# Performance work log

Hardware: AMD Instinct MI355X
Metric: run time of the kernel (lower is better)

The kernel has to match this reference:

```python
import jax, jax.numpy as jnp
import numpy as np

B, S, D, H, G = 2, 4096, 768, 12, 64
HD = D // H
W = 256              # one-sided window (attention_window=512); also the chunk size
NC = S // W
NEG = -1e9
SCALE = 1.0 / np.sqrt(HD)


def setup_inputs() -> dict:
    key = jax.random.key(0)
    ks = jax.random.split(key, 9)
    lin = lambda k: 0.02 * jax.random.normal(k, (D, D), dtype=jnp.float32)
    zb = lambda: jnp.zeros((D,), jnp.float32)
    return {
        "query": jax.random.normal(ks[0], (S, B, D), dtype=jnp.float32),
        # 0 = local token, -1 = global token (wrapper multiplies by -1 -> +1 = global in HF convention)
        "key_padding_mask": jnp.zeros((B, S), jnp.int32).at[:, :G].set(-1),
        "Wq": lin(ks[1]), "bq": zb(),
        "Wk": lin(ks[2]), "bk": zb(),
        "Wv": lin(ks[3]), "bv": zb(),
        "Wqg": lin(ks[4]), "bqg": zb(),
        "Wkg": lin(ks[5]), "bkg": zb(),
        "Wvg": lin(ks[6]), "bvg": zb(),
        "Wo": lin(ks[7]), "bo": zb(),
    }


def _heads(x):  # [B,S,D] -> [B,H,S,HD]
    return x.reshape(B, S, H, HD).transpose(0, 2, 1, 3)


def reference(query, key_padding_mask, Wq, bq, Wk, bk, Wv, bv,
              Wqg, bqg, Wkg, bkg, Wvg, bvg, Wo, bo):
    x = query.transpose(1, 0, 2)                      # [B,S,D]
    attn_mask = -key_padding_mask                     # wrapper: key_padding_mask * -1
    is_pad = attn_mask < 0                            # [B,S]
    is_glb = attn_mask > 0

    q = _heads(x @ Wq + bq) * SCALE                   # [B,H,S,HD]
    k = _heads(x @ Wk + bk)
    v = _heads(x @ Wv + bv)

    # ---- sliding-window scores via overlapping 3-chunk key blocks ----
    qc = q.reshape(B, H, NC, W, HD)
    blk_idx = jnp.arange(NC)[:, None] * W + jnp.arange(3 * W)[None, :]   # [NC,3W] into padded seq
    kpad = jnp.pad(k, ((0, 0), (0, 0), (W, W), (0, 0)))
    vpad = jnp.pad(v, ((0, 0), (0, 0), (W, W), (0, 0)))
    kblk = kpad[:, :, blk_idx]                        # [B,H,NC,3W,HD]
    vblk = vpad[:, :, blk_idx]
    local = jnp.einsum('bhcqd,bhckd->bhcqk', qc, kblk)  # [B,H,NC,W,3W]

    rel = jnp.arange(3 * W)[None, :] - jnp.arange(W)[:, None] - W        # key pos - query pos
    jpos = (jnp.arange(NC)[:, None, None] - 1) * W + jnp.arange(3 * W)[None, None, :]
    band_ok = (jnp.abs(rel)[None] <= W) & (jpos >= 0) & (jpos < S)       # [NC,W,3W]

    key_bad = is_pad | is_glb                         # pad keys masked; global keys handled separately
    kb_blk = jnp.pad(key_bad, ((0, 0), (W, W)), constant_values=True)[:, blk_idx]  # [B,NC,3W]
    ok = band_ok[None, None] & ~kb_blk[:, None, :, None, :]
    local = jnp.where(ok, local, NEG)

    # ---- all queries -> global keys (first G tokens), regular K/V ----
    gsc = jnp.einsum('bhqd,bhgd->bhqg', q, k[:, :, :G])                  # [B,H,S,G]

    scores = jnp.concatenate([gsc, local.reshape(B, H, S, 3 * W)], axis=-1)
    probs = jax.nn.softmax(scores, axis=-1)
    pg = probs[..., :G]
    pl = probs[..., G:].reshape(B, H, NC, W, 3 * W)

    out = jnp.einsum('bhcqk,bhckd->bhcqd', pl, vblk).reshape(B, H, S, HD)
    out = out + jnp.einsum('bhqg,bhgd->bhqd', pg, v[:, :, :G])

    # ---- global query rows: full attention with the dedicated global projections ----
    qg = (_heads(x @ Wqg + bqg) * SCALE)[:, :, :G]    # [B,H,G,HD]
    kg = _heads(x @ Wkg + bkg)
    vg = _heads(x @ Wvg + bvg)
    gq = jnp.einsum('bhgd,bhkd->bhgk', qg, kg)        # [B,H,G,S]
    gq = jnp.where(is_pad[:, None, None, :], NEG, gq)
    gp = jax.nn.softmax(gq, axis=-1)
    out = out.at[:, :, :G].set(jnp.einsum('bhgk,bhkd->bhgd', gp, vg))

    attn_out = out.transpose(0, 2, 1, 3).reshape(B, S, D)   # merge heads -> [B,S,D]
    attn_out = attn_out.transpose(1, 0, 2)                  # back to [S,B,D]
    return attn_out @ Wo + bo                               # wrapper's output Linear
```

## Files before the change

kernel.cpp:

```cpp
#include <hip/hip_runtime.h>
#include <hip/hip_bf16.h>
#include <cstdint>

#define BB 2
#define SS 4096
#define DD 768
#define HH 12
#define GG 64
#define WW 256

typedef __hip_bfloat16 bf16;
typedef unsigned short u16;
typedef __attribute__((ext_vector_type(8))) short short8v;
typedef __attribute__((ext_vector_type(4))) float floatx4;
typedef __attribute__((ext_vector_type(16))) float floatx16;

#define QSCALE 0.18033688011112042f

__device__ __forceinline__ float b2f(u16 u) {
  return __uint_as_float(((unsigned int)u) << 16);
}
__device__ __forceinline__ u16 f2bu(float f) {
  bf16 h = __float2bfloat16(f);
  return *reinterpret_cast<u16*>(&h);
}
__device__ __forceinline__ void async_copy16(const u16* g, u16* l) {
  __builtin_amdgcn_global_load_lds(
      (const __attribute__((address_space(1))) void*)g,
      (__attribute__((address_space(3))) void*)l, 16, 0, 0);
}

struct P7 { const void* p[7]; };

__global__ __launch_bounds__(256) void detect_dtype(const u16* __restrict__ q,
                                                    int* __restrict__ flag) {
  __shared__ int cnt;
  int tid = threadIdx.x;
  if (tid == 0) cnt = 0;
  __syncthreads();
  int bad = 0;
#pragma unroll
  for (int i = 0; i < 16; ++i) {
    float f = b2f(q[tid * 16 + i]);
    if (!isfinite(f) || fabsf(f) > 100.f) bad++;
  }
  atomicAdd(&cnt, bad);
  __syncthreads();
  if (tid == 0) *flag = (cnt > 256) ? 1 : 0;
}

__global__ __launch_bounds__(256) void prep(P7 wsrc, P7 bsrc,
                                            const void* __restrict__ qsrc,
                                            bf16* __restrict__ cWt,
                                            bf16* __restrict__ cB,
                                            bf16* __restrict__ cQ,
                                            const int* __restrict__ flag) {
  bool f32 = (*flag != 0);
  int z = blockIdx.z;
  if (z < 7) {
    __shared__ float tile[32][33];
    const void* src = wsrc.p[z];
    bf16* d = cWt + (size_t)z * DD * DD;
    int tx = threadIdx.x & 31, ty = threadIdx.x >> 5;
    int k0 = blockIdx.x * 32, n0 = blockIdx.y * 32;
#pragma unroll
    for (int i = 0; i < 32; i += 8) {
      int k = k0 + ty + i, n = n0 + tx;
      float v = f32 ? ((const float*)src)[(size_t)k * DD + n]
                    : b2f(((const u16*)src)[(size_t)k * DD + n]);
      tile[ty + i][tx] = v;
    }
    __syncthreads();
#pragma unroll
    for (int i = 0; i < 32; i += 8) {
      int n = n0 + ty + i, k = k0 + tx;
      d[(size_t)n * DD + k] = __float2bfloat16(tile[tx][ty + i]);
    }
  } else if (z == 7) {
    int bidx = blockIdx.x + 24 * blockIdx.y;
    const int nch = (BB * HH * SS * 64) / 8;
    u16* cQp = (u16*)cQ;
    for (int c = bidx * 256 + threadIdx.x; c < nch; c += 576 * 256) {
      int i = c * 8;
      if (f32) {
        const float* qs = (const float*)qsrc;
        float4 a = *(const float4*)(qs + i);
        float4 b = *(const float4*)(qs + i + 4);
        ushort4 o1 = make_ushort4(f2bu(a.x), f2bu(a.y), f2bu(a.z), f2bu(a.w));
        ushort4 o2 = make_ushort4(f2bu(b.x), f2bu(b.y), f2bu(b.z), f2bu(b.w));
        *(ushort4*)(cQp + i) = o1;
        *(ushort4*)(cQp + i + 4) = o2;
      } else {
        const u16* qs = (const u16*)qsrc;
        *(ushort4*)(cQp + i) = *(const ushort4*)(qs + i);
        *(ushort4*)(cQp + i + 4) = *(const ushort4*)(qs + i + 4);
      }
    }
  } else {
    int which = blockIdx.x;
    if (which >= 7 || blockIdx.y != 0) return;
    const void* s = bsrc.p[which];
    for (int j = threadIdx.x; j < DD; j += 256)
      cB[which * DD + j] =
          __float2bfloat16(f32 ? ((const float*)s)[j] : b2f(((const u16*)s)[j]));
  }
}

__device__ __forceinline__ short8v lda(u16 (*Ls)[64], int base, int lane, int kk) {
  int row = base + (lane & 31);
  int c = (kk >> 3) + (lane >> 5);
  return *(const short8v*)&Ls[row][((c ^ (row & 7)) << 3)];
}

__device__ __forceinline__ void gemm_core2(const u16* __restrict__ Xp,
                                           const u16* __restrict__ Wp, int bm,
                                           int bn, int tid, u16 (*As)[64],
                                           u16 (*Bs)[64], floatx16 (&acc)[2][2]) {
  int lane = tid & 63, w = tid >> 6;
  int wm = (w >> 1) * 64, wn = (w & 1) * 64;
  int r8 = lane >> 3;
  int sw = (((lane & 7) ^ (r8 & 7)) << 3);
  for (int k0 = 0; k0 < DD; k0 += 64) {
    __syncthreads();
#pragma unroll
    for (int j = 0; j < 4; ++j) {
      async_copy16(Wp + (size_t)(bn + w * 32 + j * 8 + r8) * DD + k0 + sw,
                   &As[w * 32 + j * 8][0]);
      async_copy16(Xp + (size_t)(bm + w * 32 + j * 8 + r8) * DD + k0 + sw,
                   &Bs[w * 32 + j * 8][0]);
    }
    __syncthreads();
#pragma unroll
    for (int kk = 0; kk < 64; kk += 16) {
      short8v a0 = lda(As, wn, lane, kk);
      short8v a1 = lda(As, wn + 32, lane, kk);
      short8v b0 = lda(Bs, wm, lane, kk);
      short8v b1 = lda(Bs, wm + 32, lane, kk);
      acc[0][0] = __builtin_amdgcn_mfma_f32_32x32x16_bf16(a0, b0, acc[0][0], 0, 0, 0);
      acc[0][1] = __builtin_amdgcn_mfma_f32_32x32x16_bf16(a0, b1, acc[0][1], 0, 0, 0);
      acc[1][0] = __builtin_amdgcn_mfma_f32_32x32x16_bf16(a1, b0, acc[1][0], 0, 0, 0);
      acc[1][1] = __builtin_amdgcn_mfma_f32_32x32x16_bf16(a1, b1, acc[1][1], 0, 0, 0);
    }
  }
}

__global__ __launch_bounds__(256, 4) void gemm5c(const bf16* __restrict__ Xb,
                                                 const bf16* __restrict__ Wt0,
                                                 const bf16* __restrict__ bset,
                                                 bf16* __restrict__ out0,
                                                 bf16* __restrict__ qgp) {
  __shared__ __align__(16) u16 SH[16384];
  u16 (*As)[64] = (u16(*)[64])SH;
  u16 (*Bs)[64] = (u16(*)[64])(SH + 8192);
  int tid = threadIdx.x, lane = tid & 63, w = tid >> 6;
  int orig = blockIdx.x;
  const int NWG = 5 * 384 + 6, qq = NWG >> 3, rr = NWG & 7;
  int xcd = orig & 7, idx = orig >> 3;
  int wg = (xcd < rr ? xcd * (qq + 1) : rr * (qq + 1) + (xcd - rr) * qq) + idx;
  int which, bm, bn;
  if (wg >= 1920) {
    which = 5; bm = 0; bn = (wg - 1920) * 128;
  } else {
    which = wg / 384;
    int rem = wg % 384;
    bm = (rem / 6) * 128;
    bn = (rem % 6) * 128;
  }
  const u16* Wp = (const u16*)Wt0 + (size_t)which * DD * DD;
  const u16* bias = (const u16*)bset + which * DD;
  int Sdim = (which == 5) ? GG : SS;
  u16* outp = (which == 5) ? (u16*)qgp
                           : (u16*)out0 + (size_t)which * BB * HH * SS * 64;
  float scale = (which == 0 || which == 5) ? QSCALE : 1.f;

  floatx16 acc[2][2];
#pragma unroll
  for (int i = 0; i < 2; ++i)
#pragma unroll
    for (int j = 0; j < 2; ++j) acc[i][j] = (floatx16)(0.f);
  gemm_core2((const u16*)Xb, Wp, bm, bn, tid, As, Bs, acc);

  if (which == 2 || which == 4) {
    const int TST = 132;
    u16* Ct = SH;
    int h0 = bn >> 6;
    int wm = (w >> 1) * 64;
    int wnl = w & 1;
    int s0 = bm >> 1;
#pragma unroll
    for (int p = 0; p < 2; ++p) {
      __syncthreads();
      if (wnl == p) {
#pragma unroll
        for (int nt = 0; nt < 2; ++nt)
#pragma unroll
          for (int mt = 0; mt < 2; ++mt)
#pragma unroll
            for (int g = 0; g < 4; ++g) {
              int ncl = nt * 32 + g * 8 + ((lane >> 5) << 2);
              ushort4 bi = *(const ushort4*)&bias[bn + p * 64 + ncl];
              int mrow = wm + mt * 32 + (lane & 31);
              Ct[(ncl + 0) * TST + mrow] = f2bu(acc[nt][mt][4 * g + 0] + b2f(bi.x));
              Ct[(ncl + 1) * TST + mrow] = f2bu(acc[nt][mt][4 * g + 1] + b2f(bi.y));
              Ct[(ncl + 2) * TST + mrow] = f2bu(acc[nt][mt][4 * g + 2] + b2f(bi.z));
              Ct[(ncl + 3) * TST + mrow] = f2bu(acc[nt][mt][4 * g + 3] + b2f(bi.w));
            }
      }
      __syncthreads();
#pragma unroll
      for (int j = 0; j < 4; ++j) {
        int c = j * 256 + tid;
        int ch = c & 7, rrow = c >> 3;
        int d = rrow >> 1, b = rrow & 1;
        const u16* row = &Ct[d * TST + b];
        ushort4 o1, o2;
        o1.x = row[(ch * 8 + 0) << 1];
        o1.y = row[(ch * 8 + 1) << 1];
        o1.z = row[(ch * 8 + 2) << 1];
        o1.w = row[(ch * 8 + 3) << 1];
        o2.x = row[(ch * 8 + 4) << 1];
        o2.y = row[(ch * 8 + 5) << 1];
        o2.z = row[(ch * 8 + 6) << 1];
        o2.w = row[(ch * 8 + 7) << 1];
        u16* dst = outp + ((size_t)(b * HH + h0 + p)) * (SS * 64) +
                   (size_t)d * SS + s0 + ch * 8;
        *(ushort4*)dst = o1;
        *(ushort4*)(dst + 4) = o2;
      }
    }
    return;
  }

  const int CST = 132;
  u16* Cs = SH;
  int wn = (w & 1) << 6, wmh = (w >> 1) << 5;
#pragma unroll
  for (int mt = 0; mt < 2; ++mt) {
    __syncthreads();
#pragma unroll
    for (int nt = 0; nt < 2; ++nt)
#pragma unroll
      for (int g = 0; g < 4; ++g) {
        int ncol = wn + nt * 32 + g * 8 + ((lane >> 5) << 2);
        ushort4 bi = *(const ushort4*)&bias[bn + ncol];
        int crow = wmh + (lane & 31);
        ushort4 o;
        o.x = f2bu((acc[nt][mt][4 * g + 0] + b2f(bi.x)) * scale);
        o.y = f2bu((acc[nt][mt][4 * g + 1] + b2f(bi.y)) * scale);
        o.z = f2bu((acc[nt][mt][4 * g + 2] + b2f(bi.z)) * scale);
        o.w = f2bu((acc[nt][mt][4 * g + 3] + b2f(bi.w)) * scale);
        *(ushort4*)&Cs[crow * CST + ncol] = o;
      }
    __syncthreads();
#pragma unroll
    for (int j = 0; j < 8; ++j) {
      int c = j * 256 + tid;
      int ch = c & 15, mh = c >> 4;
      int mloc = mh >> 1, hloc = mh & 1;
      int m = bm + ((mloc >> 5) << 6) + mt * 32 + (mloc & 31);
      int s = m >> 1, b = m & 1;
      int h = (bn >> 6) + hloc;
      ushort4 vv = *(const ushort4*)&Cs[mloc * CST + hloc * 64 + ch * 4];
      *(ushort4*)(outp + ((size_t)(b * HH + h) * Sdim + s) * 64 + ch * 4) = vv;
    }
  }
}

__global__ __launch_bounds__(256, 4) void gemm_out(const bf16* __restrict__ Xb,
                                                   const bf16* __restrict__ Wtb,
                                                   const bf16* __restrict__ biasb,
                                                   float* __restrict__ outv) {
  __shared__ __align__(16) u16 SH[16384];
  u16 (*As)[64] = (u16(*)[64])SH;
  u16 (*Bs)[64] = (u16(*)[64])(SH + 8192);
  float* Cf = (float*)SH;
  int tid = threadIdx.x, lane = tid & 63, w = tid >> 6;
  int wn = (w & 1) * 64;
  int orig = blockIdx.x;
  int wg = (orig & 7) * 48 + (orig >> 3);
  int bm = (wg / 6) * 128, bn = (wg % 6) * 128;
  floatx16 acc[2][2];
#pragma unroll
  for (int i = 0; i < 2; ++i)
#pragma unroll
    for (int j = 0; j < 2; ++j) acc[i][j] = (floatx16)(0.f);
  gemm_core2((const u16*)Xb, (const u16*)Wtb, bm, bn, tid, As, Bs, acc);
  const u16* bias = (const u16*)biasb;
#pragma unroll
  for (int p = 0; p < 2; ++p) {
    __syncthreads();
    if ((w >> 1) == p) {
#pragma unroll
      for (int mt = 0; mt < 2; ++mt) {
        int mloc = mt * 32 + (lane & 31);
#pragma unroll
        for (int nt = 0; nt < 2; ++nt)
#pragma unroll
          for (int g = 0; g < 4; ++g) {
            int nl = wn + nt * 32 + g * 8 + ((lane >> 5) << 2);
            ushort4 bi = *(const ushort4*)&bias[bn + nl];
            float4 o;
            o.x = acc[nt][mt][4 * g + 0] + b2f(bi.x);
            o.y = acc[nt][mt][4 * g + 1] + b2f(bi.y);
            o.z = acc[nt][mt][4 * g + 2] + b2f(bi.z);
            o.w = acc[nt][mt][4 * g + 3] + b2f(bi.w);
            int n4 = nl >> 2;
            *(float4*)&Cf[mloc * 128 + ((n4 ^ (mloc & 31)) << 2)] = o;
          }
      }
    }
    __syncthreads();
#pragma unroll
    for (int j = 0; j < 8; ++j) {
      int c = j * 256 + tid;
      int mloc = c >> 5, nch = c & 31;
      float4 v = *(const float4*)&Cf[mloc * 128 + ((nch ^ (mloc & 31)) << 2)];
      *(float4*)(outv + (size_t)(bm + p * 64 + mloc) * DD + bn + nch * 4) = v;
    }
  }
}

__global__ __launch_bounds__(256, 3) void attn_local128(
    const bf16* __restrict__ qb, const bf16* __restrict__ kb,
    const bf16* __restrict__ vtb, const int* __restrict__ kpm,
    bf16* __restrict__ attnout) {
  __shared__ __align__(16) u16 Qs[128][64];
  __shared__ __align__(16) u16 Ks[64][64];
  __shared__ __align__(16) u16 Vt[64][64];
  __shared__ __align__(16) u16 Ps[128][72];
  __shared__ float Ls[128];
  __shared__ int kbadS[64];
  int bid = blockIdx.x;
  int tile = bid & 31, bh = bid >> 5;
  int b = bh / HH, h = bh % HH;
  int tid = threadIdx.x, lane = tid & 63, w = tid >> 6;
  int quad = lane >> 4, t = lane & 15;
  const u16* qp = (const u16*)qb + (size_t)bh * SS * 64;
  const u16* kp = (const u16*)kb + (size_t)bh * SS * 64;
  const u16* vp = (const u16*)vtb + (size_t)bh * SS * 64;
  int sq0 = GG + tile * 128;
#pragma unroll
  for (int j = 0; j < 4; ++j) {
    int qr = sq0 + w * 32 + j * 8 + (lane >> 3);
    int sr = qr < SS ? qr : SS - 1;
    async_copy16(qp + (size_t)sr * 64 + (lane & 7) * 8, &Qs[w * 32 + j * 8][0]);
  }
  __syncthreads();
  short8v aq[2][2];
#pragma unroll
  for (int st = 0; st < 2; ++st)
#pragma unroll
    for (int ks = 0; ks < 2; ++ks)
      aq[st][ks] = *(const short8v*)&Qs[w * 32 + st * 16 + t][ks * 32 + quad * 8];
  floatx4 O[2][4];
#pragma unroll
  for (int st = 0; st < 2; ++st)
#pragma unroll
    for (int dt = 0; dt < 4; ++dt) O[st][dt] = (floatx4)(0.f);
  float ps[2][4] = {};
  int win_lo = max(sq0 - WW, GG);
  int win_hi = min(sq0 + 127 + WW, SS - 1);
  int kb_lo = win_lo & ~63;
  int iters = ((win_hi - kb_lo) >> 6) + 2;
  for (int it = 0; it < iters; ++it) {
    int kbs = (it == 0) ? 0 : kb_lo + ((it - 1) << 6);
    __syncthreads();
#pragma unroll
    for (int j = 0; j < 2; ++j) {
      async_copy16(kp + (size_t)(kbs + w * 16 + j * 8 + (lane >> 3)) * 64 +
                       (lane & 7) * 8,
                   &Ks[w * 16 + j * 8][0]);
      async_copy16(vp + (size_t)(w * 16 + j * 8 + (lane >> 3)) * SS + kbs +
                       (lane & 7) * 8,
                   &Vt[w * 16 + j * 8][0]);
    }
    if (tid < 64) kbadS[tid] = kpm[b * SS + kbs + tid];
    __syncthreads();
#pragma unroll
    for (int st = 0; st < 2; ++st) {
      floatx4 S[4];
#pragma unroll
      for (int nt = 0; nt < 4; ++nt) {
        S[nt] = (floatx4)(0.f);
#pragma unroll
        for (int ks = 0; ks < 2; ++ks) {
          short8v bk = *(const short8v*)&Ks[nt * 16 + t][ks * 32 + quad * 8];
          S[nt] = __builtin_amdgcn_mfma_f32_16x16x32_bf16(aq[st][ks], bk, S[nt],
                                                          0, 0, 0);
        }
      }
      int prow = w * 32 + st * 16 + quad * 4;
      if (it == 0) {
#pragma unroll
        for (int nt = 0; nt < 4; ++nt)
#pragma unroll
          for (int r = 0; r < 4; ++r) {
            float p = exp2f(S[nt][r]);
            ps[st][r] += p;
            Ps[prow + r][((nt ^ quad) << 4) + t] = f2bu(p);
          }
      } else {
#pragma unroll
        for (int r = 0; r < 4; ++r) {
          int qr = sq0 + prow + r;
          int off = kbs + t + WW - qr;
#pragma unroll
          for (int nt = 0; nt < 4; ++nt) {
            int bad = kbadS[nt * 16 + t];
            unsigned u = (unsigned)(off + nt * 16);
            float p = exp2f((u <= 2 * WW && bad == 0) ? S[nt][r] : -3.0e38f);
            ps[st][r] += p;
            Ps[prow + r][((nt ^ quad) << 4) + t] = f2bu(p);
          }
        }
      }
    }
    short8v ap[2][2];
#pragma unroll
    for (int st = 0; st < 2; ++st)
#pragma unroll
      for (int ks = 0; ks < 2; ++ks) {
        int chunk = (2 * ks + (quad >> 1)) ^ ((t >> 2) & 3);
        ap[st][ks] = *(const short8v*)&Ps[w * 32 + st * 16 + t]
                                        [(chunk << 4) + ((quad & 1) << 3)];
      }
#pragma unroll
    for (int dt = 0; dt < 4; ++dt) {
#pragma unroll
      for (int ks = 0; ks < 2; ++ks) {
        short8v av = *(const short8v*)&Vt[dt * 16 + t][ks * 32 + quad * 8];
#pragma unroll
        for (int st = 0; st < 2; ++st)
          O[st][dt] = __builtin_amdgcn_mfma_f32_16x16x32_bf16(av, ap[st][ks],
                                                              O[st][dt], 0, 0, 0);
      }
    }
  }
#pragma unroll
  for (int st = 0; st < 2; ++st) {
#pragma unroll
    for (int r = 0; r < 4; ++r)
#pragma unroll
      for (int off = 1; off < 16; off <<= 1) ps[st][r] += __shfl_xor(ps[st][r], off);
    if (t == 0)
#pragma unroll
      for (int r = 0; r < 4; ++r) Ls[w * 32 + st * 16 + quad * 4 + r] = ps[st][r];
  }
#pragma unroll
  for (int st = 0; st < 2; ++st) {
    int q = sq0 + w * 32 + st * 16 + t;
    if (q < SS) {
      float linv = 1.0f / Ls[w * 32 + st * 16 + t];
#pragma unroll
      for (int dt = 0; dt < 4; ++dt) {
        ushort4 o;
        o.x = f2bu(O[st][dt][0] * linv);
        o.y = f2bu(O[st][dt][1] * linv);
        o.z = f2bu(O[st][dt][2] * linv);
        o.w = f2bu(O[st][dt][3] * linv);
        *(ushort4*)((u16*)attnout + ((size_t)q * BB + b) * DD + h * 64 +
                    dt * 16 + quad * 4) = o;
      }
    }
  }
}

__global__ __launch_bounds__(256) void attn_glb(
    const bf16* __restrict__ qgb, const bf16* __restrict__ kgb,
    const bf16* __restrict__ vtb, const int* __restrict__ kpm,
    float* __restrict__ part) {
  __shared__ __align__(16) u16 Qs[64][72];
  __shared__ __align__(16) u16 Ks[64][72];
  __shared__ __align__(16) u16 Vt[64][72];
  __shared__ __align__(16) u16 Ps[64][72];
  __shared__ int kbadS[64];
  int bid = blockIdx.x;
  int bh = bid >> 4, seg = bid & 15;
  int b = bh / HH;
  int tid = threadIdx.x, lane = tid & 63, w = tid >> 6;
  int quad = lane >> 4, t = lane & 15;
  const u16* qp = (const u16*)qgb + (size_t)bh * GG * 64;
  const u16* kp = (const u16*)kgb + (size_t)bh * SS * 64;
  const u16* vp = (const u16*)vtb + (size_t)bh * SS * 64;
  int srow = tid >> 2, scol = (tid & 3) * 16;
#pragma unroll
  for (int i = 0; i < 4; ++i)
    *(ushort4*)&Qs[srow][scol + 4 * i] =
        *(const ushort4*)(qp + (size_t)srow * 64 + scol + 4 * i);
  __syncthreads();
  short8v aq[2];
#pragma unroll
  for (int ks = 0; ks < 2; ++ks)
    aq[ks] = *(const short8v*)&Qs[16 * w + t][ks * 32 + quad * 8];
  floatx4 O[4];
#pragma unroll
  for (int i = 0; i < 4; ++i) O[i] = (floatx4)(0.f);
  float ps[4] = {0.f, 0.f, 0.f, 0.f};
  for (int it = 0; it < 4; ++it) {
    int kbs = (seg << 8) + (it << 6);
    ushort4 ku[4], vu[4];
#pragma unroll
    for (int i = 0; i < 4; ++i) {
      ku[i] = *(const ushort4*)(kp + (size_t)(kbs + srow) * 64 + scol + 4 * i);
      vu[i] = *(const ushort4*)(vp + (size_t)srow * SS + kbs + scol + 4 * i);
    }
    int kbval = (tid < 64) ? kpm[b * SS + kbs + tid] : 0;
    __syncthreads();
#pragma unroll
    for (int i = 0; i < 4; ++i) {
      *(ushort4*)&Ks[srow][scol + 4 * i] = ku[i];
      *(ushort4*)&Vt[srow][scol + 4 * i] = vu[i];
    }
    if (tid < 64) kbadS[tid] = kbval;
    __syncthreads();
    floatx4 S[4];
#pragma unroll
    for (int nt = 0; nt < 4; ++nt) {
      S[nt] = (floatx4)(0.f);
#pragma unroll
      for (int ks = 0; ks < 2; ++ks) {
        short8v bk = *(const short8v*)&Ks[nt * 16 + t][ks * 32 + quad * 8];
        S[nt] = __builtin_amdgcn_mfma_f32_16x16x32_bf16(aq[ks], bk, S[nt], 0, 0, 0);
      }
    }
#pragma unroll
    for (int nt = 0; nt < 4; ++nt) {
      int bad = kbadS[nt * 16 + t];
#pragma unroll
      for (int r = 0; r < 4; ++r) {
        float p = exp2f((bad <= 0) ? S[nt][r] : -3.0e38f);
        ps[r] += p;
        Ps[16 * w + quad * 4 + r][((nt ^ quad) << 4) + t] = f2bu(p);
      }
    }
    short8v ap[2];
#pragma unroll
    for (int ks = 0; ks < 2; ++ks) {
      int chunk = (2 * ks + (quad >> 1)) ^ ((t >> 2) & 3);
      ap[ks] = *(const short8v*)&Ps[16 * w + t][(chunk << 4) + ((quad & 1) << 3)];
    }
#pragma unroll
    for (int dt = 0; dt < 4; ++dt)
#pragma unroll
      for (int ks = 0; ks < 2; ++ks) {
        short8v bv = *(const short8v*)&Vt[dt * 16 + t][ks * 32 + quad * 8];
        O[dt] = __builtin_amdgcn_mfma_f32_16x16x32_bf16(ap[ks], bv, O[dt], 0, 0, 0);
      }
  }
#pragma unroll
  for (int r = 0; r < 4; ++r)
#pragma unroll
    for (int off = 1; off < 16; off <<= 1) ps[r] += __shfl_xor(ps[r], off);
  float* pO = part + (size_t)bid * 4160;
#pragma unroll
  for (int dt = 0; dt < 4; ++dt)
#pragma unroll
    for (int r = 0; r < 4; ++r)
      pO[(16 * w + quad * 4 + r) * 64 + dt * 16 + t] = O[dt][r];
  if (t == 0)
#pragma unroll
    for (int r = 0; r < 4; ++r) pO[4096 + 16 * w + quad * 4 + r] = ps[r];
}

__global__ __launch_bounds__(256) void attn_comb(const float* __restrict__ part,
                                                 bf16* __restrict__ attnout) {
  int tid = threadIdx.x, lane = tid & 63, w = tid >> 6;
  int idx = blockIdx.x * 4 + w;
  int bh = idx >> 6, row = idx & 63;
  int b = bh / HH, h = bh % HH;
  float o = 0.f, L = 0.f;
#pragma unroll
  for (int s16 = 0; s16 < 16; ++s16) {
    const float* p = part + (size_t)(bh * 16 + s16) * 4160;
    o += p[(row << 6) + lane];
    L += p[4096 + row];
  }
  attnout[((size_t)row * BB + b) * DD + h * 64 + lane] = __float2bfloat16(o / L);
}

extern "C" void kernel_launch(void* const* d_in, const int* in_sizes, int n_in,
                              void* d_out, int out_size, void* d_ws,
                              size_t ws_size, hipStream_t stream) {
  const int* kpm = (const int*)d_in[1];
  float* outp = (float*)d_out;
  const size_t SZ = (size_t)BB * HH * SS * 64;
  const size_t WSZ = (size_t)DD * DD;
  bf16* p = (bf16*)d_ws;
  bf16* cQ = p; p += SZ;
  bf16* cWt = p; p += 7 * WSZ;
  bf16* cB = p; p += 7 * DD;
  bf16* q = p; p += SZ;
  bf16* k = p; p += SZ;
  bf16* v = p; p += SZ;
  bf16* kg = p; p += SZ;
  bf16* vg = p; p += SZ;
  bf16* qg = p; p += (size_t)BB * HH * GG * 64;
  bf16* attnout = p; p += SZ;
  float* part = (float*)p;
  int* flag = (int*)(part + (size_t)384 * 4160);
  dim3 blk(256);

  P7 wsrc{{d_in[2], d_in[4], d_in[6], d_in[10], d_in[12], d_in[8], d_in[14]}};
  P7 bsrc{{d_in[3], d_in[5], d_in[7], d_in[11], d_in[13], d_in[9], d_in[15]}};

  detect_dtype<<<1, blk, 0, stream>>>((const u16*)d_in[0], flag);
  prep<<<dim3(24, 24, 9), blk, 0, stream>>>(wsrc, bsrc, d_in[0], cWt, cB, cQ, flag);
  gemm5c<<<dim3(5 * 384 + 6), blk, 0, stream>>>(cQ, cWt, cB, q, qg);
  attn_local128<<<dim3(24 * 32), blk, 0, stream>>>(q, k, v, kpm, attnout);
  attn_glb<<<dim3(BB * HH * 16), blk, 0, stream>>>(qg, kg, vg, kpm, part);
  attn_comb<<<dim3(BB * HH * 16), blk, 0, stream>>>(part, attnout);
  gemm_out<<<dim3(384), blk, 0, stream>>>(attnout, cWt + 6 * WSZ, cB + 6 * DD, outp);
}
```

Baseline: 262.4 us.

## Split projection GEMM tile across 8 waves instead of 4

The fused 5-way projection GEMM now runs with 512 threads per block. Each of the 8 waves computes a 32x64 sub-tile with 2 MFMA accumulators, where previously each of 4 waves held a 64x64 sub-tile with 4 accumulators. The goal is more waves to hide latency and lower register pressure per wave. The trade-off is that B-operand LDS reads are duplicated across waves, and the epilogue is reworked into two passes to fit the new wave-to-tile mapping.

```diff
diff --git a/kernel.cpp b/kernel.cpp
--- a/kernel.cpp
+++ b/kernel.cpp
@@ -111,6 +111,12 @@
   int c = (kk >> 3) + (lane >> 5);
   return *(const short8v*)&Ls[row][((c ^ (row & 7)) << 3)];
 }
+__device__ __forceinline__ short8v ldaf(const u16* Ls, int rowbase, int lane,
+                                        int kk) {
+  int row = rowbase + (lane & 31);
+  int c = (kk >> 3) + (lane >> 5);
+  return *(const short8v*)&Ls[row * 64 + ((c ^ (row & 7)) << 3)];
+}
 
 __device__ __forceinline__ void gemm_core2(const u16* __restrict__ Xp,
                                            const u16* __restrict__ Wp, int bm,
@@ -144,15 +150,18 @@
   }
 }
 
-__global__ __launch_bounds__(256, 4) void gemm5c(const bf16* __restrict__ Xb,
+__global__ __launch_bounds__(512, 4) void gemm5d(const bf16* __restrict__ Xb,
                                                  const bf16* __restrict__ Wt0,
                                                  const bf16* __restrict__ bset,
                                                  bf16* __restrict__ out0,
                                                  bf16* __restrict__ qgp) {
   __shared__ __align__(16) u16 SH[16384];
-  u16 (*As)[64] = (u16(*)[64])SH;
-  u16 (*Bs)[64] = (u16(*)[64])(SH + 8192);
+  u16* As = SH;
+  u16* Bs = SH + 8192;
   int tid = threadIdx.x, lane = tid & 63, w = tid >> 6;
+  int wn = (w & 1) << 6, wq = w >> 1;
+  int r8 = lane >> 3;
+  int sw = (((lane & 7) ^ r8) << 3);
   int orig = blockIdx.x;
   const int NWG = 5 * 384 + 6, qq = NWG >> 3, rr = NWG & 7;
   int xcd = orig & 7, idx = orig >> 3;
@@ -166,6 +175,7 @@
     bm = (rem / 6) * 128;
     bn = (rem % 6) * 128;
   }
+  const u16* Xp = (const u16*)Xb;
   const u16* Wp = (const u16*)Wt0 + (size_t)which * DD * DD;
   const u16* bias = (const u16*)bset + which * DD;
   int Sdim = (which == 5) ? GG : SS;
@@ -173,43 +183,56 @@
                            : (u16*)out0 + (size_t)which * BB * HH * SS * 64;
   float scale = (which == 0 || which == 5) ? QSCALE : 1.f;
 
-  floatx16 acc[2][2];
-#pragma unroll
-  for (int i = 0; i < 2; ++i)
-#pragma unroll
-    for (int j = 0; j < 2; ++j) acc[i][j] = (floatx16)(0.f);
-  gemm_core2((const u16*)Xb, Wp, bm, bn, tid, As, Bs, acc);
+  floatx16 acc[2];
+  acc[0] = (floatx16)(0.f);
+  acc[1] = (floatx16)(0.f);
+
+  for (int k0 = 0; k0 < DD; k0 += 64) {
+    __syncthreads();
+#pragma unroll
+    for (int j = 0; j < 2; ++j) {
+      async_copy16(Wp + (size_t)(bn + w * 16 + j * 8 + r8) * DD + k0 + sw,
+                   As + (w * 16 + j * 8) * 64);
+      async_copy16(Xp + (size_t)(bm + w * 16 + j * 8 + r8) * DD + k0 + sw,
+                   Bs + (w * 16 + j * 8) * 64);
+    }
+    __syncthreads();
+#pragma unroll
+    for (int kk = 0; kk < 64; kk += 16) {
+      short8v a0 = ldaf(As, wn, lane, kk);
+      short8v a1 = ldaf(As, wn + 32, lane, kk);
+      short8v b0 = ldaf(Bs, wq * 32, lane, kk);
+      acc[0] = __builtin_amdgcn_mfma_f32_32x32x16_bf16(a0, b0, acc[0], 0, 0, 0);
+      acc[1] = __builtin_amdgcn_mfma_f32_32x32x16_bf16(a1, b0, acc[1], 0, 0, 0);
+    }
+  }
 
   if (which == 2 || which == 4) {
     const int TST = 132;
     u16* Ct = SH;
     int h0 = bn >> 6;
-    int wm = (w >> 1) * 64;
-    int wnl = w & 1;
     int s0 = bm >> 1;
 #pragma unroll
     for (int p = 0; p < 2; ++p) {
       __syncthreads();
-      if (wnl == p) {
+      if ((w & 1) == p) {
+        int mrow = wq * 32 + (lane & 31);
 #pragma unroll
         for (int nt = 0; nt < 2; ++nt)
 #pragma unroll
-          for (int mt = 0; mt < 2; ++mt)
-#pragma unroll
-            for (int g = 0; g < 4; ++g) {
-              int ncl = nt * 32 + g * 8 + ((lane >> 5) << 2);
-              ushort4 bi = *(const ushort4*)&bias[bn + p * 64 + ncl];
-              int mrow = wm + mt * 32 + (lane & 31);
-              Ct[(ncl + 0) * TST + mrow] = f2bu(acc[nt][mt][4 * g + 0] + b2f(bi.x));
-              Ct[(ncl + 1) * TST + mrow] = f2bu(acc[nt][mt][4 * g + 1] + b2f(bi.y));
-              Ct[(ncl + 2) * TST + mrow] = f2bu(acc[nt][mt][4 * g + 2] + b2f(bi.z));
-              Ct[(ncl + 3) * TST + mrow] = f2bu(acc[nt][mt][4 * g + 3] + b2f(bi.w));
-            }
+          for (int g = 0; g < 4; ++g) {
+            int ncl = nt * 32 + g * 8 + ((lane >> 5) << 2);
+            ushort4 bi = *(const ushort4*)&bias[bn + p * 64 + ncl];
+            Ct[(ncl + 0) * TST + mrow] = f2bu(acc[nt][4 * g + 0] + b2f(bi.x));
+            Ct[(ncl + 1) * TST + mrow] = f2bu(acc[nt][4 * g + 1] + b2f(bi.y));
+            Ct[(ncl + 2) * TST + mrow] = f2bu(acc[nt][4 * g + 2] + b2f(bi.z));
+            Ct[(ncl + 3) * TST + mrow] = f2bu(acc[nt][4 * g + 3] + b2f(bi.w));
+          }
       }
       __syncthreads();
 #pragma unroll
-      for (int j = 0; j < 4; ++j) {
-        int c = j * 256 + tid;
+      for (int j = 0; j < 2; ++j) {
+        int c = j * 512 + tid;
         int ch = c & 7, rrow = c >> 3;
         int d = rrow >> 1, b = rrow & 1;
         const u16* row = &Ct[d * TST + b];
@@ -233,31 +256,32 @@
 
   const int CST = 132;
   u16* Cs = SH;
-  int wn = (w & 1) << 6, wmh = (w >> 1) << 5;
-#pragma unroll
-  for (int mt = 0; mt < 2; ++mt) {
-    __syncthreads();
-#pragma unroll
-    for (int nt = 0; nt < 2; ++nt)
-#pragma unroll
-      for (int g = 0; g < 4; ++g) {
-        int ncol = wn + nt * 32 + g * 8 + ((lane >> 5) << 2);
-        ushort4 bi = *(const ushort4*)&bias[bn + ncol];
-        int crow = wmh + (lane & 31);
-        ushort4 o;
-        o.x = f2bu((acc[nt][mt][4 * g + 0] + b2f(bi.x)) * scale);
-        o.y = f2bu((acc[nt][mt][4 * g + 1] + b2f(bi.y)) * scale);
-        o.z = f2bu((acc[nt][mt][4 * g + 2] + b2f(bi.z)) * scale);
-        o.w = f2bu((acc[nt][mt][4 * g + 3] + b2f(bi.w)) * scale);
-        *(ushort4*)&Cs[crow * CST + ncol] = o;
-      }
-    __syncthreads();
-#pragma unroll
-    for (int j = 0; j < 8; ++j) {
-      int c = j * 256 + tid;
+#pragma unroll
+  for (int p = 0; p < 2; ++p) {
+    __syncthreads();
+    if ((wq & 1) == p) {
+      int crow = (wq >> 1) * 32 + (lane & 31);
+#pragma unroll
+      for (int nt = 0; nt < 2; ++nt)
+#pragma unroll
+        for (int g = 0; g < 4; ++g) {
+          int ncol = wn + nt * 32 + g * 8 + ((lane >> 5) << 2);
+          ushort4 bi = *(const ushort4*)&bias[bn + ncol];
+          ushort4 o;
+          o.x = f2bu((acc[nt][4 * g + 0] + b2f(bi.x)) * scale);
+          o.y = f2bu((acc[nt][4 * g + 1] + b2f(bi.y)) * scale);
+          o.z = f2bu((acc[nt][4 * g + 2] + b2f(bi.z)) * scale);
+          o.w = f2bu((acc[nt][4 * g + 3] + b2f(bi.w)) * scale);
+          *(ushort4*)&Cs[crow * CST + ncol] = o;
+        }
+    }
+    __syncthreads();
+#pragma unroll
+    for (int j = 0; j < 4; ++j) {
+      int c = j * 512 + tid;
       int ch = c & 15, mh = c >> 4;
       int mloc = mh >> 1, hloc = mh & 1;
-      int m = bm + ((mloc >> 5) << 6) + mt * 32 + (mloc & 31);
+      int m = bm + ((mloc >> 5) << 6) + p * 32 + (mloc & 31);
       int s = m >> 1, b = m & 1;
       int h = (bn >> 6) + hloc;
       ushort4 vv = *(const ushort4*)&Cs[mloc * CST + hloc * 64 + ch * 4];
@@ -605,7 +629,7 @@
 
   detect_dtype<<<1, blk, 0, stream>>>((const u16*)d_in[0], flag);
   prep<<<dim3(24, 24, 9), blk, 0, stream>>>(wsrc, bsrc, d_in[0], cWt, cB, cQ, flag);
-  gemm5c<<<dim3(5 * 384 + 6), blk, 0, stream>>>(cQ, cWt, cB, q, qg);
+  gemm5d<<<dim3(5 * 384 + 6), dim3(512), 0, stream>>>(cQ, cWt, cB, q, qg);
   attn_local128<<<dim3(24 * 32), blk, 0, stream>>>(q, k, v, kpm, attnout);
   attn_glb<<<dim3(BB * HH * 16), blk, 0, stream>>>(qg, kg, vg, kpm, part);
   attn_comb<<<dim3(BB * HH * 16), blk, 0, stream>>>(part, attnout);
```

Result: no change. 267.5 us (+2.0%).
